# Kernel optimization log

Measured on AMD Instinct MI355X. Metric: run time of the kernel, lower is better.

The kernel has to match this reference:

```python
import jax, jax.numpy as jnp
import numpy as np

N, E, IN_DIM, H, D = 100000, 1600000, 128, 4, 32


def setup_inputs() -> dict:
    key = jax.random.key(0)
    ks = jax.random.split(key, 8)
    glorot = lambda k, shape: jax.random.uniform(
        k, shape, jnp.float32, -1.0, 1.0) * np.sqrt(6.0 / (shape[0] + shape[1]))
    return {
        "x": jax.random.normal(ks[0], (N, IN_DIM), jnp.float32),
        "row": jax.random.randint(ks[1], (E,), 0, N, jnp.int32),
        "col": jax.random.randint(ks[2], (E,), 0, N, jnp.int32),
        "W_l": glorot(ks[3], (IN_DIM, H * D)),
        "W_r": glorot(ks[4], (IN_DIM, H * D)),
        "a1w": glorot(ks[5], (IN_DIM, H)),
        "a2w": glorot(ks[6], (IN_DIM, H)),
        "bias": jnp.zeros((H * D,), jnp.float32),
    }


def reference(x, row, col, W_l, W_r, a1w, a2w, bias):
    n = x.shape[0]  # num_nodes (= graph[0].max()+1 with dense random rows)
    x_l = (x @ W_l).reshape(n, H, D)          # [N,H,D]
    x_r = x @ W_r                              # [N,H*D]
    # per-edge attention logits: a1[row] + a2[col], leaky-relu(0.2)
    attn = jax.nn.leaky_relu((x @ a1w)[row] + (x @ a2w)[col], 0.2)  # [E,H]
    # segment softmax over destination rows (numerically stable)
    m = jax.ops.segment_max(attn, row, num_segments=n)               # [N,H]
    e = jnp.exp(attn - m[row])
    s = jax.ops.segment_sum(e, row, num_segments=n)                  # [N,H]
    attn_d = e / s[row]                                              # [E,H]
    # per-head SpMM: scatter-add weighted source features to destinations
    msgs = attn_d[:, :, None] * x_l[col]                             # [E,H,D]
    out = jax.ops.segment_sum(msgs, row, num_segments=n).reshape(n, H * D)
    return out + x_r + bias
```

## Files before the change

### kernel.cpp

```cpp
#include <hip/hip_runtime.h>


typedef short bfvec8 __attribute__((ext_vector_type(8)));
typedef float f32x4  __attribute__((ext_vector_type(4)));

#define BK 128
#define CAPC 3584
#define EPB 2048
#define REC 256
#define BSTR 16

__device__ __forceinline__ unsigned short f2bf(float f) {
  union { float f; unsigned int i; } v; v.f = f;
  unsigned int r = v.i + 0x7fffu + ((v.i >> 16) & 1u);
  return (unsigned short)(r >> 16);
}

__global__ __launch_bounds__(128) void wprep_k(
    const float* __restrict__ Wl, const float* __restrict__ Wr,
    const float* __restrict__ a1w, const float* __restrict__ a2w,
    unsigned short* __restrict__ Wtg, int* __restrict__ bcur, int NBK)
{
  const int n = blockIdx.x;
  const int y = blockIdx.y;
  const int k = threadIdx.x;
  if (y == 0 && n < 8) {
    int b = n * 128 + k;
    if (b < NBK) bcur[b * BSTR] = b * CAPC;
  }
  const float* W = y ? Wr : Wl;
  const float LOG2E = 1.4426950408889634f;
  float v;
  if (n < 128)      v = W[(size_t)k * 128 + n];
  else if (y)       v = 0.f;
  else if (n < 132) v = a1w[k * 4 + (n - 128)] * LOG2E;
  else              v = a2w[k * 4 + (n - 132)] * LOG2E;
  Wtg[((size_t)y * 136 + n) * 128 + k] = f2bf(v);
}

__global__ __launch_bounds__(256) void gemm_bin_k(
    const float* __restrict__ x, const unsigned short* __restrict__ Wtg,
    const float* __restrict__ bias,
    char* __restrict__ xls, float* __restrict__ out,
    float* __restrict__ s1, float* __restrict__ s2, int N,
    const int* __restrict__ row, const int* __restrict__ col,
    int* __restrict__ bcur, unsigned int* __restrict__ binned,
    int E, int NBK, int binBlocks, int gemmBlocks)
{
  __shared__ __align__(16) char raw[52224];
  const int bid = blockIdx.x;
  const int t = threadIdx.x;
  const bool isbin = (bid % 3 == 0) && (bid / 3 < binBlocks);

  if (isbin) {
    int* h    = (int*)raw;
    int* base = (int*)(raw + 4096);
    const int sub = bid / 3;
    const int e0 = sub * EPB;
    const int e1 = min(e0 + EPB, E);

    int rloc[8];
    for (int i = t; i < NBK; i += 256) h[i] = 0;
    __syncthreads();
    #pragma unroll
    for (int k = 0; k < 8; ++k) {
      int e = e0 + t + (k << 8);
      rloc[k] = (e < e1) ? row[e] : -1;
      if (rloc[k] >= 0) atomicAdd(&h[rloc[k] >> 7], 1);
    }
    __syncthreads();
    for (int i = t; i < NBK; i += 256) {
      int c = h[i];
      base[i] = c ? atomicAdd(&bcur[i * BSTR], c) : 0;
    }
    __syncthreads();
    for (int i = t; i < NBK; i += 256) h[i] = 0;
    __syncthreads();
    #pragma unroll
    for (int k = 0; k < 8; ++k) {
      int e = e0 + t + (k << 8);
      if (e < e1) {
        int r = rloc[k];
        unsigned c = (unsigned)col[e];
        int b = r >> 7;
        int rk = atomicAdd(&h[b], 1);
        binned[base[b] + rk] = ((unsigned)(r & 127) << 17) | c;
      }
    }
    return;
  }

  unsigned short (*xs)[136] = (unsigned short(*)[136])raw;
  unsigned short (*Ws)[136] = (unsigned short(*)[136])(raw + 64*272);
  const int sub = bid - min(bid / 3 + 1, binBlocks);
  if (sub >= gemmBlocks) return;
  const int n0 = sub * 64;

  for (int i = t; i < 2048; i += 256) {
    int rr = i >> 5, kc = (i & 31) << 2;
    float4 v = make_float4(0.f, 0.f, 0.f, 0.f);
    int n = n0 + rr;
    if (n < N) v = *(const float4*)&x[(size_t)n * 128 + kc];
    unsigned int lo = (unsigned int)f2bf(v.x) | ((unsigned int)f2bf(v.y) << 16);
    unsigned int hi = (unsigned int)f2bf(v.z) | ((unsigned int)f2bf(v.w) << 16);
    *(uint2*)&xs[rr][kc] = make_uint2(lo, hi);
  }

  const int w    = t >> 6;
  const int lane = t & 63;
  const int m    = lane & 15;
  const int quad = lane >> 4;

  bfvec8 afr[4];
  {
    int arow = 128 + (m < 8 ? m : 7);
    #pragma unroll
    for (int kc4 = 0; kc4 < 4; ++kc4)
      afr[kc4] = *(const bfvec8*)&Wtg[(size_t)arow * 128 + kc4 * 32 + quad * 8];
  }

  const int nrow = n0 + 16 * w + m;

  #pragma unroll
  for (int y = 0; y < 2; ++y) {
    const unsigned short* Wt = Wtg + (size_t)y * 136 * 128;
    if (y) __syncthreads();
    for (int i = t; i < 2048; i += 256) {
      int nr = i >> 4, kc = (i & 15) << 3;
      *(uint4*)&Ws[nr][kc] = *(const uint4*)&Wt[(size_t)nr * 128 + kc];
    }
    __syncthreads();

    f32x4 acc[9];
    #pragma unroll
    for (int i = 0; i < 9; ++i) acc[i] = (f32x4){0.f, 0.f, 0.f, 0.f};

    #pragma unroll
    for (int kc4 = 0; kc4 < 4; ++kc4) {
      const int kc = kc4 * 32;
      bfvec8 af = *(const bfvec8*)&xs[16 * w + m][kc + quad * 8];
      #pragma unroll
      for (int nt = 0; nt < 8; ++nt) {
        bfvec8 bfr = *(const bfvec8*)&Ws[nt * 16 + m][kc + quad * 8];
        acc[nt] = __builtin_amdgcn_mfma_f32_16x16x32_bf16(bfr, af, acc[nt], 0, 0, 0);
      }
      if (y == 0)
        acc[8] = __builtin_amdgcn_mfma_f32_16x16x32_bf16(afr[kc4], af, acc[8], 0, 0, 0);
    }

    if (nrow < N) {
      if (y) {
        #pragma unroll
        for (int nt = 0; nt < 8; ++nt) {
          int c = nt * 16 + quad * 4;
          float4 b4 = *(const float4*)&bias[c];
          float4 v = make_float4(acc[nt][0] + b4.x, acc[nt][1] + b4.y,
                                 acc[nt][2] + b4.z, acc[nt][3] + b4.w);
          *(float4*)&out[(size_t)nrow * 128 + c] = v;
        }
      } else {
        #pragma unroll
        for (int nt = 0; nt < 8; ++nt) {
          int c = nt * 16 + quad * 4;
          unsigned lo = (unsigned)f2bf(acc[nt][0]) | ((unsigned)f2bf(acc[nt][1]) << 16);
          unsigned hi = (unsigned)f2bf(acc[nt][2]) | ((unsigned)f2bf(acc[nt][3]) << 16);
          *(uint2*)(xls + ((size_t)nrow << 8) + 2 * c) = make_uint2(lo, hi);
        }
        if (quad == 0) *(f32x4*)&s1[nrow * 4] = acc[8];
        else if (quad == 1) *(f32x4*)&s2[nrow * 4] = acc[8];
      }
    }
  }
}

__global__ __launch_bounds__(256) void csr_k(const unsigned int* __restrict__ binned,
    const int* __restrict__ bcur, int* __restrict__ offs, int* __restrict__ deg,
    unsigned int* __restrict__ colsort, int N)
{
  __shared__ unsigned ecache[CAPC];
  __shared__ int h[BK];
  __shared__ int sh[BK];
  const int t = threadIdx.x;
  const int b = blockIdx.x;
  const int lo = b * BK;
  const int e0 = b * CAPC;
  const int e1 = bcur[b * BSTR];

  if (t < BK) h[t] = 0;
  __syncthreads();
  for (int i = e0 + t; i < e1; i += 256) {
    unsigned p = binned[i];
    ecache[i - e0] = p;
    atomicAdd(&h[p >> 17], 1);
  }
  __syncthreads();

  int v = 0;
  if (t < BK) { v = h[t]; sh[t] = v; }
  __syncthreads();
  for (int off = 1; off < BK; off <<= 1) {
    int tv = (t < BK && t >= off) ? sh[t - off] : 0;
    __syncthreads();
    if (t < BK) sh[t] += tv;
    __syncthreads();
  }
  if (t < BK) {
    int ex = sh[t] - v;
    int node = lo + t;
    if (node < N) { offs[node] = e0 + ex; deg[node] = v; }
    h[t] = ex;
  }
  __syncthreads();
  const int cnt = e1 - e0;
  for (int i = t; i < cnt; i += 256) {
    unsigned p = ecache[i];
    int rlo = p >> 17;
    unsigned c = p & 0x1FFFFu;
    int pos = atomicAdd(&h[rlo], 1);
    colsort[e0 + pos] = c << 8;
  }
}

__global__ __launch_bounds__(256) void agg_k(const int* __restrict__ offs,
    const int* __restrict__ deg, const unsigned int* __restrict__ colsort,
    const float* __restrict__ s1, const float* __restrict__ s2,
    const char* __restrict__ xls, float* __restrict__ out, int N)
{
  const int lane = threadIdx.x & 63;
  const int n = blockIdx.x * 4 + (threadIdx.x >> 6);
  if (n >= N) return;
  const int e0 = offs[n], e1 = e0 + deg[n];
  const int h  = lane >> 4;
  const int hp = lane & 3;
  const int jj = (lane >> 2) & 7;
  const float s1c = s1[n * 4 + hp];
  const unsigned lane4 = (unsigned)(lane << 2);
  const unsigned hp4   = (unsigned)(hp << 2);
  const char* s2b = (const char*)s2;

  float acc0 = 0.f, acc1 = 0.f, wsum = 0.f;
  int i0 = e0;
  for (; i0 + 8 <= e1; i0 += 8) {
    unsigned csl = colsort[i0 + jj];
    float z2 = *(const float*)(s2b + ((csl >> 4) + hp4));
    float z = s1c + z2;
    z = fmaxf(z, 0.2f * z);
    float wv = exp2f(z);

    unsigned cs[8];
    #pragma unroll
    for (int j = 0; j < 8; ++j) cs[j] = colsort[i0 + j];
    unsigned pv[8];
    #pragma unroll
    for (int j = 0; j < 8; ++j)
      pv[j] = *(const unsigned*)(xls + (cs[j] + lane4));

    #pragma unroll
    for (int j = 0; j < 8; ++j) {
      float wj = __shfl(wv, (j << 2) | h);
      wsum += wj;
      union { unsigned u; float f; } lo, hi;
      lo.u = pv[j] << 16;
      hi.u = pv[j] & 0xffff0000u;
      acc0 += wj * lo.f;
      acc1 += wj * hi.f;
    }
  }
  if (i0 < e1) {
    const int rem = e1 - i0;
    unsigned csl = colsort[i0 + (jj < rem ? jj : rem - 1)];
    float z2 = *(const float*)(s2b + ((csl >> 4) + hp4));
    float z = s1c + z2;
    z = fmaxf(z, 0.2f * z);
    float wv = (jj < rem) ? exp2f(z) : 0.f;

    unsigned cs[8];
    #pragma unroll
    for (int j = 0; j < 8; ++j) cs[j] = colsort[i0 + (j < rem ? j : rem - 1)];
    unsigned pv[8];
    #pragma unroll
    for (int j = 0; j < 8; ++j)
      pv[j] = *(const unsigned*)(xls + (cs[j] + lane4));

    #pragma unroll
    for (int j = 0; j < 8; ++j) {
      float wj = __shfl(wv, (j << 2) | h);
      wsum += wj;
      union { unsigned u; float f; } lo, hi;
      lo.u = pv[j] << 16;
      hi.u = pv[j] & 0xffff0000u;
      acc0 += wj * lo.f;
      acc1 += wj * hi.f;
    }
  }

  float inv = (wsum > 0.f) ? (1.0f / wsum) : 0.f;
  const size_t o = (size_t)n * 128 + 2 * lane;
  float2 xr = *(const float2*)&out[o];
  float2 res; res.x = acc0 * inv + xr.x; res.y = acc1 * inv + xr.y;
  *(float2*)&out[o] = res;
}

extern "C" void kernel_launch(void* const* d_in, const int* in_sizes, int n_in,
                              void* d_out, int out_size, void* d_ws, size_t ws_size,
                              hipStream_t stream) {
  const float* x    = (const float*)d_in[0];
  const int*   row  = (const int*)d_in[1];
  const int*   col  = (const int*)d_in[2];
  const float* Wl   = (const float*)d_in[3];
  const float* Wr   = (const float*)d_in[4];
  const float* a1w  = (const float*)d_in[5];
  const float* a2w  = (const float*)d_in[6];
  const float* bias = (const float*)d_in[7];
  float* out = (float*)d_out;
  const int N = in_sizes[0] / 128;
  const int E = in_sizes[1];
  (void)n_in; (void)out_size; (void)ws_size;

  const int NBK = (N + BK - 1) / BK;

  char* ws = (char*)d_ws;
  size_t off = 0;
  auto carve = [&](size_t bytes) { void* p = ws + off; off += (bytes + 255) & ~(size_t)255; return p; };
  char* xls            = (char*)carve((size_t)N * REC);
  float* s1            = (float*)carve((size_t)N * 4 * 4);
  float* s2            = (float*)carve((size_t)N * 4 * 4);
  int* offs            = (int*)carve((size_t)N * 4);
  int* deg             = (int*)carve((size_t)N * 4);
  unsigned int* colsort= (unsigned int*)carve((size_t)NBK * CAPC * 4);
  unsigned int* binned = (unsigned int*)carve((size_t)NBK * CAPC * 4);
  int* bcur            = (int*)carve((size_t)NBK * BSTR * 4);
  unsigned short* Wtg  = (unsigned short*)carve((size_t)2 * 136 * 128 * 2);

  const int gemmBlocks = (N + 63) / 64;
  const int binBlocks  = (E + EPB - 1) / EPB;
  const int T = gemmBlocks + binBlocks;

  wprep_k   <<<dim3(136, 2), 128, 0, stream>>>(Wl, Wr, a1w, a2w, Wtg, bcur, NBK);
  gemm_bin_k<<<T, 256, 0, stream>>>(x, Wtg, bias, xls, out, s1, s2, N,
                                    row, col, bcur, binned, E, NBK,
                                    binBlocks, gemmBlocks);
  csr_k     <<<NBK, 256, 0, stream>>>(binned, bcur, offs, deg, colsort, N);
  agg_k     <<<(N + 3) / 4, 256, 0, stream>>>(offs, deg, colsort, s1, s2, xls, out, N);
}
```

Baseline: 269.7 us.

## Load GEMM operands directly from global into registers, drop LDS staging

```diff
diff --git a/kernel.cpp b/kernel.cpp
--- a/kernel.cpp
+++ b/kernel.cpp
@@ -47,14 +47,13 @@
     int* __restrict__ bcur, unsigned int* __restrict__ binned,
     int E, int NBK, int binBlocks, int gemmBlocks)
 {
-  __shared__ __align__(16) char raw[52224];
+  __shared__ int h[1024];
+  __shared__ int base[1024];
   const int bid = blockIdx.x;
   const int t = threadIdx.x;
   const bool isbin = (bid % 3 == 0) && (bid / 3 < binBlocks);
 
   if (isbin) {
-    int* h    = (int*)raw;
-    int* base = (int*)(raw + 4096);
     const int sub = bid / 3;
     const int e0 = sub * EPB;
     const int e1 = min(e0 + EPB, E);
@@ -90,46 +89,40 @@
     return;
   }
 
-  unsigned short (*xs)[136] = (unsigned short(*)[136])raw;
-  unsigned short (*Ws)[136] = (unsigned short(*)[136])(raw + 64*272);
   const int sub = bid - min(bid / 3 + 1, binBlocks);
   if (sub >= gemmBlocks) return;
   const int n0 = sub * 64;
-
-  for (int i = t; i < 2048; i += 256) {
-    int rr = i >> 5, kc = (i & 31) << 2;
-    float4 v = make_float4(0.f, 0.f, 0.f, 0.f);
-    int n = n0 + rr;
-    if (n < N) v = *(const float4*)&x[(size_t)n * 128 + kc];
-    unsigned int lo = (unsigned int)f2bf(v.x) | ((unsigned int)f2bf(v.y) << 16);
-    unsigned int hi = (unsigned int)f2bf(v.z) | ((unsigned int)f2bf(v.w) << 16);
-    *(uint2*)&xs[rr][kc] = make_uint2(lo, hi);
-  }
 
   const int w    = t >> 6;
   const int lane = t & 63;
   const int m    = lane & 15;
   const int quad = lane >> 4;
-
-  bfvec8 afr[4];
-  {
-    int arow = 128 + (m < 8 ? m : 7);
-    #pragma unroll
-    for (int kc4 = 0; kc4 < 4; ++kc4)
-      afr[kc4] = *(const bfvec8*)&Wtg[(size_t)arow * 128 + kc4 * 32 + quad * 8];
-  }
-
   const int nrow = n0 + 16 * w + m;
+  const int kb   = quad * 8;
+
+  bfvec8 afx[4];
+  #pragma unroll
+  for (int kc4 = 0; kc4 < 4; ++kc4) {
+    f32x4 u = (f32x4){0.f, 0.f, 0.f, 0.f};
+    f32x4 v = (f32x4){0.f, 0.f, 0.f, 0.f};
+    if (nrow < N) {
+      const float* xp = &x[(size_t)nrow * 128 + kc4 * 32 + kb];
+      u = *(const f32x4*)xp;
+      v = *(const f32x4*)(xp + 4);
+    }
+    bfvec8 a;
+    a[0] = (short)f2bf(u[0]); a[1] = (short)f2bf(u[1]);
+    a[2] = (short)f2bf(u[2]); a[3] = (short)f2bf(u[3]);
+    a[4] = (short)f2bf(v[0]); a[5] = (short)f2bf(v[1]);
+    a[6] = (short)f2bf(v[2]); a[7] = (short)f2bf(v[3]);
+    afx[kc4] = a;
+  }
+
+  const int arow = 128 + (m < 8 ? m : 7);
 
   #pragma unroll
   for (int y = 0; y < 2; ++y) {
     const unsigned short* Wt = Wtg + (size_t)y * 136 * 128;
-    if (y) __syncthreads();
-    for (int i = t; i < 2048; i += 256) {
-      int nr = i >> 4, kc = (i & 15) << 3;
-      *(uint4*)&Ws[nr][kc] = *(const uint4*)&Wt[(size_t)nr * 128 + kc];
-    }
-    __syncthreads();
 
     f32x4 acc[9];
     #pragma unroll
@@ -137,15 +130,16 @@
 
     #pragma unroll
     for (int kc4 = 0; kc4 < 4; ++kc4) {
-      const int kc = kc4 * 32;
-      bfvec8 af = *(const bfvec8*)&xs[16 * w + m][kc + quad * 8];
+      const int kc = kc4 * 32 + kb;
       #pragma unroll
       for (int nt = 0; nt < 8; ++nt) {
-        bfvec8 bfr = *(const bfvec8*)&Ws[nt * 16 + m][kc + quad * 8];
-        acc[nt] = __builtin_amdgcn_mfma_f32_16x16x32_bf16(bfr, af, acc[nt], 0, 0, 0);
+        bfvec8 bfr = *(const bfvec8*)&Wt[(size_t)(nt * 16 + m) * 128 + kc];
+        acc[nt] = __builtin_amdgcn_mfma_f32_16x16x32_bf16(bfr, afx[kc4], acc[nt], 0, 0, 0);
       }
-      if (y == 0)
-        acc[8] = __builtin_amdgcn_mfma_f32_16x16x32_bf16(afr[kc4], af, acc[8], 0, 0, 0);
+      if (y == 0) {
+        bfvec8 ar = *(const bfvec8*)&Wt[(size_t)arow * 128 + kc];
+        acc[8] = __builtin_amdgcn_mfma_f32_16x16x32_bf16(ar, afx[kc4], acc[8], 0, 0, 0);
+      }
     }
 
     if (nrow < N) {
```

After: 290.5 us. 1.08x slower.
